# Performance work log

Hardware: AMD Instinct MI355X
Metric: run time of the kernel (lower is better)

The kernel has to match this reference:

```python
import jax, jax.numpy as jnp
import numpy as np

KS = 3
N = KS * KS
LN_EPS = 1e-5


def conv2d(x, w, stride=1, pad=0):
    return jax.lax.conv_general_dilated(
        x, w, (stride, stride), [(pad, pad), (pad, pad)],
        dimension_numbers=('NCHW', 'OIHW', 'NCHW'))


def layer_norm(x, g, b):
    mu = jnp.mean(x, axis=-1, keepdims=True)
    var = jnp.mean(jnp.square(x - mu), axis=-1, keepdims=True)
    return (x - mu) * jax.lax.rsqrt(var + LN_EPS) * g + b


def l2norm(x):
    n = jnp.sqrt(jnp.sum(jnp.square(x), axis=-1, keepdims=True))
    return x / jnp.maximum(n, 1e-12)


def deform_conv(x, w_p, b_p, w_d):
    # canonical DeformConv2d (kernel 3, pad 1, stride 1, no modulation)
    B, C, H, W = x.shape
    off = conv2d(x, w_p, stride=1, pad=1) + b_p[None, :, None, None]  # [B,2N,H,W]
    xp = jnp.pad(x, ((0, 0), (0, 0), (1, 1), (1, 1)))
    Hp, Wp = H + 2, W + 2
    pn = jnp.stack(jnp.meshgrid(jnp.arange(-1, 2), jnp.arange(-1, 2), indexing='ij'), 0)
    pn = pn.reshape(2, N).astype(x.dtype)  # kernel offsets, row-major (dx,dy)
    p0x = jnp.arange(1, H + 1, dtype=x.dtype)
    p0y = jnp.arange(1, W + 1, dtype=x.dtype)
    # sampling coords, [B,H,W,N]
    px = off[:, :N].transpose(0, 2, 3, 1) + p0x[None, :, None, None] + pn[0][None, None, None, :]
    py = off[:, N:].transpose(0, 2, 3, 1) + p0y[None, None, :, None] + pn[1][None, None, None, :]
    fx = jnp.floor(px)
    fy = jnp.floor(py)
    qlx = jnp.clip(fx, 0, Hp - 1)
    qly = jnp.clip(fy, 0, Wp - 1)
    qrx = jnp.clip(fx + 1, 0, Hp - 1)
    qry = jnp.clip(fy + 1, 0, Wp - 1)
    pxc = jnp.clip(px, 0, Hp - 1)
    pyc = jnp.clip(py, 0, Wp - 1)
    g_lt = (1 + (qlx - pxc)) * (1 + (qly - pyc))
    g_rb = (1 - (qrx - pxc)) * (1 - (qry - pyc))
    g_lb = (1 + (qlx - pxc)) * (1 - (qry - pyc))
    g_rt = (1 - (qrx - pxc)) * (1 + (qly - pyc))
    xf = xp.reshape(B, C, Hp * Wp)

    def gat(ix, iy):
        idx = (ix.astype(jnp.int32) * Wp + iy.astype(jnp.int32)).reshape(B, 1, -1)
        g = jnp.take_along_axis(xf, jnp.broadcast_to(idx, (B, C, idx.shape[-1])), axis=2)
        return g.reshape(B, C, H, W, N)

    xo = (g_lt[:, None] * gat(qlx, qly) + g_rb[:, None] * gat(qrx, qry)
          + g_lb[:, None] * gat(qlx, qry) + g_rt[:, None] * gat(qrx, qly))
    # [B,C,H,W,N] -> [B,C,H*ks,W*ks] (row = h*ks+kr, col = w*ks+kc)
    xo = xo.reshape(B, C, H, W, KS, KS).transpose(0, 1, 2, 4, 3, 5).reshape(B, C, H * KS, W * KS)
    return conv2d(xo, w_d, stride=KS, pad=0)


def setup_inputs() -> dict:
    key = jax.random.key(0)
    ks = jax.random.split(key, 8)
    B, C, H, W, heads = 4, 192, 64, 64, 6
    hid = 4 * C
    return {
        'x': jax.random.normal(ks[0], (B, C, H, W), dtype=jnp.float32),
        'gamma1': jnp.ones((C,), jnp.float32),
        'beta1': jnp.zeros((C,), jnp.float32),
        'gamma2': jnp.ones((C,), jnp.float32),
        'beta2': jnp.zeros((C,), jnp.float32),
        'temperature': jnp.ones((heads, 1, 1), jnp.float32),
        'w_qkv': jax.random.normal(ks[1], (3 * C, C), jnp.float32) * 0.02,
        'w_proj': jax.random.normal(ks[2], (C, C), jnp.float32) * 0.02,
        'w_p': jax.random.normal(ks[3], (2 * N, C, KS, KS), jnp.float32) * 0.01,
        'b_p': jnp.zeros((2 * N,), jnp.float32),
        'w_d': jax.random.normal(ks[4], (C, C, KS, KS), jnp.float32) * 0.02,
        'w_fc1': jax.random.normal(ks[5], (C, hid), jnp.float32) * 0.02,
        'b_fc1': jnp.zeros((hid,), jnp.float32),
        'w_fc2': jax.random.normal(ks[6], (hid, C), jnp.float32) * 0.02,
        'b_fc2': jnp.zeros((C,), jnp.float32),
    }


def reference(x, gamma1, beta1, gamma2, beta2, temperature, w_qkv, w_proj,
              w_p, b_p, w_d, w_fc1, b_fc1, w_fc2, b_fc2):
    B, C, H, W = x.shape
    heads = temperature.shape[0]
    xs = x.reshape(B, C, H * W).transpose(0, 2, 1)  # [B,HW,C]
    shortcut = xs
    xn = layer_norm(xs, gamma1, beta1).transpose(0, 2, 1).reshape(B, C, H, W)
    # SSA: deformable-conv query + channel attention over C
    q = deform_conv(xn, w_p, b_p, w_d)
    qkv = jnp.einsum('bchw,oc->bohw', xn, w_qkv)
    k_spe, v_spe = qkv[:, C:2 * C], qkv[:, 2 * C:]

    def split(t):
        return t.reshape(B, heads, C // heads, H * W)

    qh = split(q)
    kh = l2norm(split(k_spe))
    vh = l2norm(split(v_spe))
    attn = jnp.einsum('bhcn,bhdn->bhcd', qh, kh) * temperature[None]
    attn = jax.nn.softmax(attn, axis=-1)
    out = jnp.einsum('bhcd,bhdn->bhcn', attn, vh).reshape(B, C, H, W)
    out = jnp.einsum('bchw,oc->bohw', out, w_proj)
    xs2 = shortcut + out.reshape(B, C, H * W).transpose(0, 2, 1)
    h1 = layer_norm(xs2, gamma2, beta2)
    m = jax.nn.gelu(h1 @ w_fc1 + b_fc1, approximate=False) @ w_fc2 + b_fc2
    xs3 = xs2 + m
    return xs3.transpose(0, 2, 1).reshape(B, C, H, W)
```

## Files before the change

### kernel.cpp

```cpp
#include <hip/hip_runtime.h>
#include <math.h>

typedef unsigned short u16;
typedef unsigned int u32;
typedef short s16x8 __attribute__((ext_vector_type(8)));
typedef float f32x4 __attribute__((ext_vector_type(4)));

#define AS1 __attribute__((address_space(1)))
#define AS3 __attribute__((address_space(3)))

__device__ __forceinline__ float bf2f(u16 u) {
    union { u32 i; float f; } v; v.i = ((u32)u) << 16; return v.f;
}
__device__ __forceinline__ u16 f2bf(float f) {
    union { float f; u32 i; } v; v.f = f;
    u32 r = v.i + 0x7fffu + ((v.i >> 16) & 1u);
    return (u16)(r >> 16);
}
__device__ __forceinline__ void gll16(const u16* g, u16* l) {
    __builtin_amdgcn_global_load_lds((const AS1 u32*)g, (AS3 u32*)l, 16, 0, 0);
}

__global__ void prep_kernel(const float* __restrict__ wd, const float* __restrict__ wqkv,
                            const float* __restrict__ wfc1, const float* __restrict__ wfc2,
                            const float* __restrict__ wp,
                            u16* __restrict__ wdT, u16* __restrict__ wkvT,
                            u16* __restrict__ wf1T, u16* __restrict__ wf2T,
                            u16* __restrict__ wpT)
{
    int i = blockIdx.x * 256 + threadIdx.x;
    if (i < 331776) {
        int o = i / 1728, r = i % 1728;
        int p = r / 192, c = r % 192;
        int cs = c ^ ((o & 7) << 3);
        wdT[(p * 192 + o) * 192 + cs] = f2bf(wd[(o * 192 + c) * 9 + p]);
    }
    if (i < 73728) {
        int o = i / 192, c = i % 192;
        wkvT[i] = f2bf(wqkv[(192 + o) * 192 + c]);
    }
    if (i < 147456) {
        int n = i / 192, c = i % 192;
        wf1T[i] = f2bf(wfc1[c * 768 + n]);
        int n2 = i / 768, hh = i % 768;
        wf2T[i] = f2bf(wfc2[hh * 192 + n2]);
    }
    if (i < 31104) {
        int n = i / 1728, r = i % 1728;
        int p = r / 192, c = r % 192;
        wpT[i] = f2bf(wp[(n * 192 + c) * 9 + p]);
    } else if (i < 55296) {
        wpT[i] = 0;
    }
}

__global__ __launch_bounds__(256) void ln1_kernel(const float* __restrict__ x,
                                                  const float* __restrict__ g,
                                                  const float* __restrict__ be,
                                                  u16* __restrict__ xn)
{
    __shared__ float red0[256], red1[256];
    __shared__ float mu_s[64], rs_s[64];
    __shared__ float xt[64 * 193];
    __shared__ u16 tile[64 * 194];
    int t = threadIdx.x, tl = t & 63, cg = t >> 6;
    int m0 = blockIdx.x * 64;
    int b = m0 >> 12, hw0 = m0 & 4095;
    const float* xb = x + (size_t)b * 786432 + hw0 + tl;
    float s = 0.f, s2 = 0.f;
    for (int cc = cg; cc < 192; cc += 4) {
        float v = xb[cc * 4096];
        xt[tl * 193 + cc] = v;
        s += v; s2 += v * v;
    }
    red0[t] = s; red1[t] = s2;
    __syncthreads();
    if (t < 64) {
        float a = red0[t] + red0[64 + t] + red0[128 + t] + red0[192 + t];
        float q = red1[t] + red1[64 + t] + red1[128 + t] + red1[192 + t];
        float mu = a * (1.f / 192.f);
        float var = q * (1.f / 192.f) - mu * mu;
        mu_s[t] = mu; rs_s[t] = rsqrtf(var + 1e-5f);
    }
    __syncthreads();
    float mu = mu_s[tl], rs = rs_s[tl];
    for (int cc = cg; cc < 192; cc += 4) {
        float v = (xt[tl * 193 + cc] - mu) * rs * g[cc] + be[cc];
        tile[tl * 194 + cc] = f2bf(v);
    }
    __syncthreads();
    u32* dst = (u32*)(xn + (size_t)m0 * 192);
    for (int i = t; i < 64 * 96; i += 256) {
        int r = i / 96, c2 = i % 96;
        dst[i] = *(const u32*)&tile[r * 194 + c2 * 2];
    }
}

__global__ __launch_bounds__(256) void offconv_kernel(const u16* __restrict__ xn,
                                                      const u16* __restrict__ wpT,
                                                      const float* __restrict__ bp,
                                                      float* __restrict__ off)
{
    __shared__ u16 As[64 * 200];
    __shared__ u16 Bs[32 * 200];
    int bh = blockIdx.x;
    int b = bh >> 6, h = bh & 63;
    int t = threadIdx.x;
    int lane = t & 63, wv = t >> 6;
    f32x4 acc[2];
#pragma unroll
    for (int j = 0; j < 2; j++) { acc[j][0] = 0.f; acc[j][1] = 0.f; acc[j][2] = 0.f; acc[j][3] = 0.f; }
    int r = t >> 2, cq = (t & 3) * 48;
    for (int p = 0; p < 9; p++) {
        int dh = p / 3 - 1, dw = p % 3 - 1;
        int hr = h + dh, wr = r + dw;
        bool valid = (hr >= 0) && (hr < 64) && (wr >= 0) && (wr < 64);
        const u16* src = xn + ((size_t)(b * 4096 + hr * 64 + wr)) * 192 + cq;
#pragma unroll
        for (int j = 0; j < 6; j++) {
            s16x8 v = {0, 0, 0, 0, 0, 0, 0, 0};
            if (valid) v = *(const s16x8*)(src + j * 8);
            *(s16x8*)&As[r * 200 + cq + j * 8] = v;
        }
#pragma unroll
        for (int i = 0; i < 3; i++) {
            int q = t + i * 256;
            int n = q / 24, c8 = q % 24;
            *(s16x8*)&Bs[n * 200 + c8 * 8] =
                *(const s16x8*)(wpT + n * 1728 + p * 192 + c8 * 8);
        }
        __syncthreads();
#pragma unroll
        for (int kc = 0; kc < 6; kc++) {
            s16x8 af = *(const s16x8*)&As[(wv * 16 + (lane & 15)) * 200 + kc * 32 + (lane >> 4) * 8];
            s16x8 b0 = *(const s16x8*)&Bs[(lane & 15) * 200 + kc * 32 + (lane >> 4) * 8];
            s16x8 b1 = *(const s16x8*)&Bs[(16 + (lane & 15)) * 200 + kc * 32 + (lane >> 4) * 8];
            acc[0] = __builtin_amdgcn_mfma_f32_16x16x32_bf16(af, b0, acc[0], 0, 0, 0);
            acc[1] = __builtin_amdgcn_mfma_f32_16x16x32_bf16(af, b1, acc[1], 0, 0, 0);
        }
        __syncthreads();
    }
    int col = lane & 15;
    int wbase = wv * 16 + (lane >> 4) * 4;
#pragma unroll
    for (int j = 0; j < 2; j++) {
        int n = j * 16 + col;
        if (n < 18) {
            float bb = bp[n];
#pragma unroll
            for (int rr = 0; rr < 4; rr++) {
                int w = wbase + rr;
                off[((size_t)(b * 4096 + h * 64 + w)) * 18 + n] = acc[j][rr] + bb;
            }
        }
    }
}

__global__ __launch_bounds__(512, 2) void gemm_deform(const u16* __restrict__ xn,
                                                      const float* __restrict__ off,
                                                      const u16* __restrict__ wdT,
                                                      u16* __restrict__ qt)
{
    __shared__ u16 As[64 * 200];
    __shared__ u16 Bs[192 * 192];
    __shared__ int sidx[64][9][4];
    __shared__ float swt[64][9][4];
    int t = threadIdx.x, lane = t & 63, wv = t >> 6;
    int wm = wv & 1, wn = wv >> 1;
    int m0 = blockIdx.x * 64;
    int b = m0 >> 12;
    for (int i = t; i < 576; i += 512) {
        int mi = i / 9, p = i % 9;
        int m = m0 + mi;
        int hw = m & 4095;
        int h = hw >> 6, w = hw & 63;
        float ox = off[(size_t)m * 18 + p];
        float oy = off[(size_t)m * 18 + 9 + p];
        float px = ox + (float)(h + 1) + (float)(p / 3 - 1);
        float py = oy + (float)(w + 1) + (float)(p % 3 - 1);
        float fx = floorf(px), fy = floorf(py);
        float qlx = fminf(fmaxf(fx, 0.f), 65.f);
        float qly = fminf(fmaxf(fy, 0.f), 65.f);
        float qrx = fminf(fmaxf(fx + 1.f, 0.f), 65.f);
        float qry = fminf(fmaxf(fy + 1.f, 0.f), 65.f);
        float pxc = fminf(fmaxf(px, 0.f), 65.f);
        float pyc = fminf(fmaxf(py, 0.f), 65.f);
        float gxl = 1.f + (qlx - pxc), gxr = 1.f - (qrx - pxc);
        float gyl = 1.f + (qly - pyc), gyr = 1.f - (qry - pyc);
        int xl = (int)qlx, xr = (int)qrx, yl = (int)qly, yr = (int)qry;
        int cx[4] = {xl, xr, xl, xr};
        int cy[4] = {yl, yr, yr, yl};
        float cw[4] = {gxl * gyl, gxr * gyr, gxl * gyr, gxr * gyl};
#pragma unroll
        for (int k = 0; k < 4; k++) {
            bool ok = (cx[k] >= 1) && (cx[k] <= 64) && (cy[k] >= 1) && (cy[k] <= 64);
            sidx[mi][p][k] = ok ? (b * 4096 + (cx[k] - 1) * 64 + (cy[k] - 1)) * 192 : 0;
            swt[mi][p][k] = ok ? cw[k] : 0.f;
        }
    }
    __syncthreads();
    f32x4 acc[2][3];
#pragma unroll
    for (int i = 0; i < 2; i++)
#pragma unroll
        for (int j = 0; j < 3; j++) {
            acc[i][j][0] = 0.f; acc[i][j][1] = 0.f; acc[i][j][2] = 0.f; acc[i][j][3] = 0.f;
        }
    int mi = t >> 3, ch = (t & 7) * 24;
    int orow[3], oxr[3];
#pragma unroll
    for (int j = 0; j < 3; j++) {
        int o = wn * 48 + j * 16 + (lane & 15);
        orow[j] = o * 192;
        oxr[j] = (o & 7) << 3;
    }
    int kb0 = (lane >> 4) * 8;

    {
        const u16* bsrc = wdT;
#pragma unroll
        for (int i2 = 0; i2 < 9; i2++) {
            int jc = wv + 8 * i2;
            gll16(bsrc + jc * 512 + lane * 8, Bs + jc * 512);
        }
        const int*   si = sidx[mi][0];
        const float* sw = swt[mi][0];
        s16x8 pc[4][3];
#pragma unroll
        for (int k = 0; k < 4; k++)
#pragma unroll
            for (int s = 0; s < 3; s++)
                pc[k][s] = *(const s16x8*)(xn + si[k] + ch + s * 8);
        float v[24];
#pragma unroll
        for (int j = 0; j < 24; j++) v[j] = 0.f;
#pragma unroll
        for (int k = 0; k < 4; k++) {
            float wt = sw[k];
#pragma unroll
            for (int j = 0; j < 24; j++) v[j] += wt * bf2f((u16)pc[k][j >> 3][j & 7]);
        }
#pragma unroll
        for (int s = 0; s < 3; s++) {
            s16x8 ov;
#pragma unroll
            for (int e = 0; e < 8; e++) ov[e] = (short)f2bf(v[s * 8 + e]);
            *(s16x8*)&As[mi * 200 + ch + s * 8] = ov;
        }
        asm volatile("s_waitcnt vmcnt(0)" ::: "memory");
        __syncthreads();
    }

    for (int p = 0; p < 9; p++) {
        s16x8 nc[4][3];
        if (p < 8) {
            const int* si = sidx[mi][p + 1];
#pragma unroll
            for (int k = 0; k < 4; k++)
#pragma unroll
                for (int s = 0; s < 3; s++)
                    nc[k][s] = *(const s16x8*)(xn + si[k] + ch + s * 8);
        }
#pragma unroll
        for (int kk = 0; kk < 6; kk++) {
            int kb = kk * 32 + kb0;
            s16x8 af[2], bfr[3];
#pragma unroll
            for (int i = 0; i < 2; i++)
                af[i] = *(const s16x8*)&As[(wm * 32 + i * 16 + (lane & 15)) * 200 + kb];
#pragma unroll
            for (int j = 0; j < 3; j++)
                bfr[j] = *(const s16x8*)&Bs[orow[j] + (kb ^ oxr[j])];
#pragma unroll
            for (int i = 0; i < 2; i++)
#pragma unroll
                for (int j = 0; j < 3; j++)
                    acc[i][j] = __builtin_amdgcn_mfma_f32_16x16x32_bf16(af[i], bfr[j], acc[i][j], 0, 0, 0);
        }
        if (p < 8) {
            __syncthreads();
            const u16* bsrc = wdT + (size_t)(p + 1) * 36864;
#pragma unroll
            for (int i2 = 0; i2 < 9; i2++) {
                int jc = wv + 8 * i2;
                gll16(bsrc + jc * 512 + lane * 8, Bs + jc * 512);
            }
            const float* sw = swt[mi][p + 1];
            float v[24];
#pragma unroll
            for (int j = 0; j < 24; j++) v[j] = 0.f;
#pragma unroll
            for (int k = 0; k < 4; k++) {
                float wt = sw[k];
#pragma unroll
                for (int j = 0; j < 24; j++) v[j] += wt * bf2f((u16)nc[k][j >> 3][j & 7]);
            }
#pragma unroll
            for (int s = 0; s < 3; s++) {
                s16x8 ov;
#pragma unroll
                for (int e = 0; e < 8; e++) ov[e] = (short)f2bf(v[s * 8 + e]);
                *(s16x8*)&As[mi * 200 + ch + s * 8] = ov;
            }
            asm volatile("s_waitcnt vmcnt(0)" ::: "memory");
            __syncthreads();
        }
    }
    int col = lane & 15;
#pragma unroll
    for (int i = 0; i < 2; i++)
#pragma unroll
        for (int j = 0; j < 3; j++) {
            int mm = m0 + wm * 32 + i * 16 + (lane >> 4) * 4;
            int nn = wn * 48 + j * 16 + col;
#pragma unroll
            for (int r = 0; r < 4; r++)
                qt[(size_t)(mm + r) * 192 + nn] = f2bf(acc[i][j][r]);
        }
}

template<int BM, int BN, int WM, int WN, int EP>
__global__ __launch_bounds__((BM / WM) * (BN / WN) * 64)
void gemm_bt(const u16* __restrict__ A, int lda,
             const u16* __restrict__ B, int ldb, int bstride,
             void* __restrict__ out, int ldc,
             const float* __restrict__ ex1, int K)
{
    constexpr int BK = 32;
    constexpr int WAVES_M = BM / WM, WAVES_N = BN / WN, NW = WAVES_M * WAVES_N;
    constexpr int TM = WM / 16, TN = WN / 16;
    constexpr int NLA = BM / 16, NLB = BN / 16;
    __shared__ u16 As[BM * BK];
    __shared__ u16 Bs[BN * BK];
    int tid = threadIdx.x;
    int lane = tid & 63, wv = tid >> 6;
    int wm = wv % WAVES_M, wn = wv / WAVES_M;
    int m0 = blockIdx.x * BM, n0 = blockIdx.y * BN;
    const u16* Bp = B + (size_t)(m0 >> 12) * bstride;
    f32x4 acc[TM][TN];
#pragma unroll
    for (int i = 0; i < TM; i++)
#pragma unroll
        for (int j = 0; j < TN; j++) {
            acc[i][j][0] = 0.f; acc[i][j][1] = 0.f; acc[i][j][2] = 0.f; acc[i][j][3] = 0.f;
        }
    int arow_l = lane >> 2;
    int acol_l = (lane & 3) * 8;
    for (int k0 = 0; k0 < K; k0 += BK) {
#pragma unroll 1
        for (int j = wv; j < NLA + NLB; j += NW) {
            if (j < NLA) {
                int row = j * 16 + arow_l;
                gll16(A + (size_t)(m0 + row) * lda + k0 + acol_l, As + j * 512);
            } else {
                int row = (j - NLA) * 16 + arow_l;
                gll16(Bp + (size_t)(n0 + row) * ldb + k0 + acol_l, Bs + (j - NLA) * 512);
            }
        }
        asm volatile("s_waitcnt vmcnt(0)" ::: "memory");
        __syncthreads();
        s16x8 af[TM], bfr[TN];
#pragma unroll
        for (int i = 0; i < TM; i++)
            af[i] = *(const s16x8*)&As[(wm * WM + i * 16 + (lane & 15)) * BK + (lane >> 4) * 8];
#pragma unroll
        for (int j = 0; j < TN; j++)
            bfr[j] = *(const s16x8*)&Bs[(wn * WN + j * 16 + (lane & 15)) * BK + (lane >> 4) * 8];
#pragma unroll
        for (int i = 0; i < TM; i++)
#pragma unroll
            for (int j = 0; j < TN; j++)
                acc[i][j] = __builtin_amdgcn_mfma_f32_16x16x32_bf16(af[i], bfr[j], acc[i][j], 0, 0, 0);
        __syncthreads();
    }
    int col = lane & 15;
#pragma unroll
    for (int i = 0; i < TM; i++)
#pragma unroll
        for (int j = 0; j < TN; j++) {
            int mm = m0 + wm * WM + i * 16 + (lane >> 4) * 4;
            int nn = n0 + wn * WN + j * 16 + col;
            if (EP == 0) {
                u16* o = (u16*)out;
#pragma unroll
                for (int r = 0; r < 4; r++) o[(size_t)(mm + r) * ldc + nn] = f2bf(acc[i][j][r]);
            } else if (EP == 1) {
                float* o = (float*)out;
                const float* xr = ex1 + (size_t)(mm >> 12) * 786432 + (size_t)nn * 4096 + (mm & 4095);
#pragma unroll
                for (int r = 0; r < 4; r++) o[(size_t)(mm + r) * ldc + nn] = acc[i][j][r] + xr[r];
            } else if (EP == 2) {
                u16* o = (u16*)out;
                float bb = ex1[nn];
#pragma unroll
                for (int r = 0; r < 4; r++) {
                    float v = acc[i][j][r] + bb;
                    o[(size_t)(mm + r) * ldc + nn] = f2bf(0.5f * v * (1.f + erff(v * 0.70710678118654752f)));
                }
            } else {
                float* o = (float*)out;
                float bb = ex1[nn];
#pragma unroll
                for (int r = 0; r < 4; r++) o[(size_t)(mm + r) * ldc + nn] = acc[i][j][r] + bb;
            }
        }
}

__global__ __launch_bounds__(384) void norm_kernel(const u16* __restrict__ kv,
                                                   float* __restrict__ norm2)
{
    int b = blockIdx.y, ch = blockIdx.x;
    int t = threadIdx.x;
    const u16* base = kv + ((size_t)(b * 4096 + ch * 128)) * 384 + t;
    float s = 0.f;
    for (int r = 0; r < 128; r++) { float v = bf2f(base[(size_t)r * 384]); s += v * v; }
    atomicAdd(&norm2[b * 384 + t], s);
}

__global__ __launch_bounds__(64) void attnp_kernel(const u16* __restrict__ qt,
                                                   const u16* __restrict__ kvt,
                                                   float* __restrict__ raw)
{
    __shared__ float qT[32 * 69];
    __shared__ float kT[32 * 69];
    int ch = blockIdx.x, h = blockIdx.y, b = blockIdx.z;
    int t = threadIdx.x;
    size_t base = (size_t)(b * 4096 + ch * 64);
    for (int e = t; e < 2048; e += 64) {
        int r = e >> 5, c = e & 31;
        qT[c * 69 + r] = bf2f(qt[(base + r) * 192 + h * 32 + c]);
        kT[c * 69 + r] = bf2f(kvt[(base + r) * 384 + h * 32 + c]);
    }
    __syncthreads();
    int tc = t >> 3, td = t & 7;
    int c0 = tc * 4, d0 = td * 4;
    float acc[4][4] = {};
    for (int r = 0; r < 64; r++) {
        float qv[4], kv4[4];
#pragma unroll
        for (int u = 0; u < 4; u++) { qv[u] = qT[(c0 + u) * 69 + r]; kv4[u] = kT[(d0 + u) * 69 + r]; }
#pragma unroll
        for (int u = 0; u < 4; u++)
#pragma unroll
            for (int v = 0; v < 4; v++) acc[u][v] += qv[u] * kv4[v];
    }
    float* dst = raw + ((size_t)(b * 6 + h)) * 1024;
#pragma unroll
    for (int u = 0; u < 4; u++)
#pragma unroll
        for (int v = 0; v < 4; v++)
            atomicAdd(&dst[(c0 + u) * 32 + d0 + v], acc[u][v]);
}

__global__ __launch_bounds__(1024) void softmax_kernel(const float* __restrict__ raw,
                                                       const float* __restrict__ norm2,
                                                       const float* __restrict__ temp,
                                                       float* __restrict__ att2)
{
    int h = blockIdx.x, b = blockIdx.y;
    int t = threadIdx.x;
    int c = t >> 5, d = t & 31;
    __shared__ float invk[32], invv[32];
    if (t < 32)       invk[t] = 1.f / fmaxf(sqrtf(norm2[b * 384 + h * 32 + t]), 1e-12f);
    else if (t < 64)  invv[t - 32] = 1.f / fmaxf(sqrtf(norm2[b * 384 + 192 + h * 32 + (t - 32)]), 1e-12f);
    __syncthreads();
    float T = temp[h];
    float v = raw[((size_t)(b * 6 + h) * 32 + c) * 32 + d] * invk[d] * T;
    float mx = v;
    for (int s = 16; s > 0; s >>= 1) mx = fmaxf(mx, __shfl_xor(mx, s, 32));
    float e = expf(v - mx);
    float sm = e;
    for (int s = 16; s > 0; s >>= 1) sm += __shfl_xor(sm, s, 32);
    att2[((size_t)(b * 6 + h) * 32 + c) * 32 + d] = (e / sm) * invv[d];
}

__global__ __launch_bounds__(192) void mb_kernel(const float* __restrict__ wproj,
                                                 const float* __restrict__ att2,
                                                 u16* __restrict__ Mb)
{
    int o2 = blockIdx.x, b = blockIdx.y, t = threadIdx.x;
    int h = t >> 5, d = t & 31;
    float s = 0.f;
#pragma unroll
    for (int c = 0; c < 32; c++)
        s += wproj[o2 * 192 + h * 32 + c] * att2[((size_t)(b * 6 + h) * 32 + c) * 32 + d];
    Mb[((size_t)b * 192 + o2) * 192 + t] = f2bf(s);
}

__global__ __launch_bounds__(256) void ln2_kernel(const float* __restrict__ xs2,
                                                  const float* __restrict__ g,
                                                  const float* __restrict__ be,
                                                  u16* __restrict__ h1)
{
    int t = threadIdx.x;
    int wv = t >> 6, l = t & 63;
    size_t m = (size_t)blockIdx.x * 4 + wv;
    const float* row = xs2 + m * 192;
    float v0 = row[l], v1 = row[l + 64], v2 = row[l + 128];
    float s = v0 + v1 + v2, s2 = v0 * v0 + v1 * v1 + v2 * v2;
    for (int sh = 32; sh > 0; sh >>= 1) { s += __shfl_xor(s, sh); s2 += __shfl_xor(s2, sh); }
    float mu = s * (1.f / 192.f);
    float var = s2 * (1.f / 192.f) - mu * mu;
    float rs = rsqrtf(var + 1e-5f);
    u16* o = h1 + m * 192;
    o[l]       = f2bf((v0 - mu) * rs * g[l]       + be[l]);
    o[l + 64]  = f2bf((v1 - mu) * rs * g[l + 64]  + be[l + 64]);
    o[l + 128] = f2bf((v2 - mu) * rs * g[l + 128] + be[l + 128]);
}

__global__ __launch_bounds__(256) void final_kernel(const float* __restrict__ xs2,
                                                    const float* __restrict__ m2,
                                                    float* __restrict__ out)
{
    __shared__ float tile[192 * 65];
    int blk = blockIdx.x;
    int b = blk >> 6, hw0 = (blk & 63) * 64;
    int t = threadIdx.x;
    size_t mbase = ((size_t)b * 4096 + hw0) * 192;
    for (int i = t; i < 64 * 192; i += 256) {
        int r = i / 192, c = i % 192;
        tile[c * 65 + r] = xs2[mbase + i] + m2[mbase + i];
    }
    __syncthreads();
    for (int i = t; i < 64 * 192; i += 256) {
        int c = i / 64, r = i % 64;
        out[(size_t)b * 786432 + (size_t)c * 4096 + hw0 + r] = tile[c * 65 + r];
    }
}

extern "C" void kernel_launch(void* const* d_in, const int* in_sizes, int n_in,
                              void* d_out, int out_size, void* d_ws, size_t ws_size,
                              hipStream_t stream)
{
    const float* x      = (const float*)d_in[0];
    const float* gamma1 = (const float*)d_in[1];
    const float* beta1  = (const float*)d_in[2];
    const float* gamma2 = (const float*)d_in[3];
    const float* beta2  = (const float*)d_in[4];
    const float* temp   = (const float*)d_in[5];
    const float* w_qkv  = (const float*)d_in[6];
    const float* w_proj = (const float*)d_in[7];
    const float* w_p    = (const float*)d_in[8];
    const float* b_p    = (const float*)d_in[9];
    const float* w_d    = (const float*)d_in[10];
    const float* w_fc1  = (const float*)d_in[11];
    const float* b_fc1  = (const float*)d_in[12];
    const float* w_fc2  = (const float*)d_in[13];
    const float* b_fc2  = (const float*)d_in[14];
    float* out = (float*)d_out;
    char* ws = (char*)d_ws;

    u16*   xn    = (u16*)(ws + 0);
    float* off   = (float*)(ws + 6291456);
    u16*   adef  = (u16*)(ws + 7471104);
    u16*   wpT   = adef;
    u16*   m1    = adef;
    float* m2    = (float*)(ws + 7471104 + 25165824);
    u16*   qt    = (u16*)(ws + 64094208);
    u16*   kvt   = (u16*)(ws + 70385664);
    float* norm2 = (float*)(ws + 82968576);
    float* araw  = (float*)(ws + 82974720);
    float* att2  = (float*)(ws + 83073024);
    u16*   Mb    = (u16*)(ws + 83171328);
    float* xs2   = (float*)(ws + 83318784);
    u16*   h1    = xn;
    u16*   wdT   = (u16*)(ws + 95901696);
    u16*   wkvT  = (u16*)(ws + 96565248);
    u16*   wf1T  = (u16*)(ws + 96712704);
    u16*   wf2T  = (u16*)(ws + 97007616);

    hipMemsetAsync(norm2, 0, 6144 + 98304, stream);
    prep_kernel<<<1296, 256, 0, stream>>>(w_d, w_qkv, w_fc1, w_fc2, w_p, wdT, wkvT, wf1T, wf2T, wpT);
    ln1_kernel<<<256, 256, 0, stream>>>(x, gamma1, beta1, xn);
    offconv_kernel<<<256, 256, 0, stream>>>(xn, wpT, b_p, off);
    gemm_deform<<<256, 512, 0, stream>>>(xn, off, wdT, qt);
    gemm_bt<128, 128, 64, 64, 0><<<dim3(128, 3), 256, 0, stream>>>(xn, 192, wkvT, 192, 0, kvt, 384, nullptr, 192);
    norm_kernel<<<dim3(32, 4), 384, 0, stream>>>(kvt, norm2);
    attnp_kernel<<<dim3(64, 6, 4), 64, 0, stream>>>(qt, kvt, araw);
    softmax_kernel<<<dim3(6, 4), 1024, 0, stream>>>(araw, norm2, temp, att2);
    mb_kernel<<<dim3(192, 4), 192, 0, stream>>>(w_proj, att2, Mb);
    gemm_bt<128, 192, 64, 48, 1><<<dim3(128, 1), 512, 0, stream>>>(kvt + 192, 384, Mb, 192, 192 * 192, xs2, 192, x, 192);
    ln2_kernel<<<4096, 256, 0, stream>>>(xs2, gamma2, beta2, h1);
    gemm_bt<128, 128, 64, 64, 2><<<dim3(128, 6), 256, 0, stream>>>(h1, 192, wf1T, 192, 0, m1, 768, b_fc1, 192);
    gemm_bt<128, 192, 64, 48, 3><<<dim3(128, 1), 512, 0, stream>>>(m1, 768, wf2T, 768, 0, m2, 192, b_fc2, 768);
    final_kernel<<<256, 256, 0, stream>>>(xs2, m2, out);
}
```

Before: 270.3 us.

## Fuse norm, LayerNorm2 and final residual/transposes into GEMM epilogues; drop attention atomics

Folds the k/v squared-norm reduction into the kv GEMM epilogue and LayerNorm2 into the projection GEMM epilogue, which now uses a 64x192 tile so each block holds whole rows. The fc2 GEMM epilogue adds the residual and writes the NCHW output directly, removing the separate norm, ln2 and final transpose kernels and the m2 buffer. attnp now writes per-chunk partials instead of using atomics, and softmax sums the 64 partials. This saves launches and round trips through global memory, at the cost of heavier epilogues, strided output writes and extra partial-buffer traffic.

After: 244.3 us. 1.11x faster.

```diff
diff --git a/kernel.cpp b/kernel.cpp
--- a/kernel.cpp
+++ b/kernel.cpp
@@ -324,7 +324,10 @@
 void gemm_bt(const u16* __restrict__ A, int lda,
              const u16* __restrict__ B, int ldb, int bstride,
              void* __restrict__ out, int ldc,
-             const float* __restrict__ ex1, int K)
+             const float* __restrict__ ex1, int K,
+             const float* __restrict__ ex2,
+             const float* __restrict__ exg, const float* __restrict__ exb,
+             void* __restrict__ out2)
 {
     constexpr int BK = 32;
     constexpr int WAVES_M = BM / WM, WAVES_N = BN / WN, NW = WAVES_M * WAVES_N;
@@ -374,47 +377,142 @@
         __syncthreads();
     }
     int col = lane & 15;
-#pragma unroll
-    for (int i = 0; i < TM; i++)
-#pragma unroll
-        for (int j = 0; j < TN; j++) {
-            int mm = m0 + wm * WM + i * 16 + (lane >> 4) * 4;
-            int nn = n0 + wn * WN + j * 16 + col;
-            if (EP == 0) {
-                u16* o = (u16*)out;
+    int rg = lane >> 4;
+    if constexpr (EP == 0) {
+        u16* o = (u16*)out;
+#pragma unroll
+        for (int i = 0; i < TM; i++)
+#pragma unroll
+            for (int j = 0; j < TN; j++) {
+                int mm = m0 + wm * WM + i * 16 + rg * 4;
+                int nn = n0 + wn * WN + j * 16 + col;
 #pragma unroll
                 for (int r = 0; r < 4; r++) o[(size_t)(mm + r) * ldc + nn] = f2bf(acc[i][j][r]);
-            } else if (EP == 1) {
-                float* o = (float*)out;
-                const float* xr = ex1 + (size_t)(mm >> 12) * 786432 + (size_t)nn * 4096 + (mm & 4095);
-#pragma unroll
-                for (int r = 0; r < 4; r++) o[(size_t)(mm + r) * ldc + nn] = acc[i][j][r] + xr[r];
-            } else if (EP == 2) {
-                u16* o = (u16*)out;
+            }
+    } else if constexpr (EP == 2) {
+        u16* o = (u16*)out;
+#pragma unroll
+        for (int i = 0; i < TM; i++)
+#pragma unroll
+            for (int j = 0; j < TN; j++) {
+                int mm = m0 + wm * WM + i * 16 + rg * 4;
+                int nn = n0 + wn * WN + j * 16 + col;
                 float bb = ex1[nn];
 #pragma unroll
                 for (int r = 0; r < 4; r++) {
                     float v = acc[i][j][r] + bb;
                     o[(size_t)(mm + r) * ldc + nn] = f2bf(0.5f * v * (1.f + erff(v * 0.70710678118654752f)));
                 }
-            } else {
-                float* o = (float*)out;
+            }
+    } else if constexpr (EP == 4) {
+        __shared__ float lnA[BM][2];
+        __shared__ float lnB[BM][2];
+        float v[TM][TN][4];
+        float sr[TM][4], sq[TM][4];
+#pragma unroll
+        for (int i = 0; i < TM; i++)
+#pragma unroll
+            for (int r = 0; r < 4; r++) { sr[i][r] = 0.f; sq[i][r] = 0.f; }
+#pragma unroll
+        for (int i = 0; i < TM; i++) {
+            int mm = m0 + wm * WM + i * 16 + rg * 4;
+#pragma unroll
+            for (int j = 0; j < TN; j++) {
+                int nn = n0 + wn * WN + j * 16 + col;
+                const float* xr = ex1 + (size_t)(mm >> 12) * 786432 + (size_t)nn * 4096 + (mm & 4095);
+#pragma unroll
+                for (int r = 0; r < 4; r++) {
+                    float vv = acc[i][j][r] + xr[r];
+                    v[i][j][r] = vv;
+                    sr[i][r] += vv; sq[i][r] += vv * vv;
+                }
+            }
+        }
+#pragma unroll
+        for (int i = 0; i < TM; i++)
+#pragma unroll
+            for (int r = 0; r < 4; r++)
+#pragma unroll
+                for (int sh = 1; sh < 16; sh <<= 1) {
+                    sr[i][r] += __shfl_xor(sr[i][r], sh);
+                    sq[i][r] += __shfl_xor(sq[i][r], sh);
+                }
+        if (col == 0) {
+#pragma unroll
+            for (int i = 0; i < TM; i++)
+#pragma unroll
+                for (int r = 0; r < 4; r++) {
+                    int row = wm * WM + i * 16 + rg * 4 + r;
+                    lnA[row][wn] = sr[i][r];
+                    lnB[row][wn] = sq[i][r];
+                }
+        }
+        __syncthreads();
+        float* oxs = (float*)out;
+        u16* oh = (u16*)out2;
+#pragma unroll
+        for (int i = 0; i < TM; i++) {
+            int mm = m0 + wm * WM + i * 16 + rg * 4;
+#pragma unroll
+            for (int r = 0; r < 4; r++) {
+                int row = wm * WM + i * 16 + rg * 4 + r;
+                float tot = lnA[row][0] + lnA[row][1];
+                float tq  = lnB[row][0] + lnB[row][1];
+                float mu = tot * (1.f / 192.f);
+                float var = tq * (1.f / 192.f) - mu * mu;
+                float rstd = rsqrtf(var + 1e-5f);
+#pragma unroll
+                for (int j = 0; j < TN; j++) {
+                    int nn = n0 + wn * WN + j * 16 + col;
+                    float vv = v[i][j][r];
+                    oxs[(size_t)(mm + r) * ldc + nn] = vv;
+                    oh[(size_t)(mm + r) * ldc + nn] = f2bf((vv - mu) * rstd * exg[nn] + exb[nn]);
+                }
+            }
+        }
+    } else if constexpr (EP == 5) {
+        float* o = (float*)out;
+#pragma unroll
+        for (int i = 0; i < TM; i++)
+#pragma unroll
+            for (int j = 0; j < TN; j++) {
+                int mm = m0 + wm * WM + i * 16 + rg * 4;
+                int nn = n0 + wn * WN + j * 16 + col;
                 float bb = ex1[nn];
-#pragma unroll
-                for (int r = 0; r < 4; r++) o[(size_t)(mm + r) * ldc + nn] = acc[i][j][r] + bb;
-            }
-        }
-}
-
-__global__ __launch_bounds__(384) void norm_kernel(const u16* __restrict__ kv,
-                                                   float* __restrict__ norm2)
-{
-    int b = blockIdx.y, ch = blockIdx.x;
-    int t = threadIdx.x;
-    const u16* base = kv + ((size_t)(b * 4096 + ch * 128)) * 384 + t;
-    float s = 0.f;
-    for (int r = 0; r < 128; r++) { float v = bf2f(base[(size_t)r * 384]); s += v * v; }
-    atomicAdd(&norm2[b * 384 + t], s);
+                size_t obase = (size_t)(mm >> 12) * 786432 + (size_t)nn * 4096;
+#pragma unroll
+                for (int r = 0; r < 4; r++) {
+                    float vv = acc[i][j][r] + bb + ex2[(size_t)(mm + r) * ldc + nn];
+                    o[obase + ((mm + r) & 4095)] = vv;
+                }
+            }
+    } else if constexpr (EP == 6) {
+        u16* o = (u16*)out;
+        float* nrm = (float*)out2;
+        int bI = m0 >> 12;
+#pragma unroll
+        for (int j = 0; j < TN; j++) {
+            float s = 0.f;
+#pragma unroll
+            for (int i = 0; i < TM; i++) {
+                int mm = m0 + wm * WM + i * 16 + rg * 4;
+                int nn = n0 + wn * WN + j * 16 + col;
+#pragma unroll
+                for (int r = 0; r < 4; r++) {
+                    u16 hb = f2bf(acc[i][j][r]);
+                    o[(size_t)(mm + r) * ldc + nn] = hb;
+                    float fv = bf2f(hb);
+                    s += fv * fv;
+                }
+            }
+            s += __shfl_xor(s, 16);
+            s += __shfl_xor(s, 32);
+            if (rg == 0) {
+                int nn = n0 + wn * WN + j * 16 + col;
+                atomicAdd(&nrm[bI * 384 + nn], s);
+            }
+        }
+    }
 }
 
 __global__ __launch_bounds__(64) void attnp_kernel(const u16* __restrict__ qt,
@@ -444,12 +542,12 @@
 #pragma unroll
             for (int v = 0; v < 4; v++) acc[u][v] += qv[u] * kv4[v];
     }
-    float* dst = raw + ((size_t)(b * 6 + h)) * 1024;
+    float* dst = raw + (((size_t)(b * 6 + h) * 64 + ch) * 1024);
 #pragma unroll
     for (int u = 0; u < 4; u++)
 #pragma unroll
         for (int v = 0; v < 4; v++)
-            atomicAdd(&dst[(c0 + u) * 32 + d0 + v], acc[u][v]);
+            dst[(c0 + u) * 32 + d0 + v] = acc[u][v];
 }
 
 __global__ __launch_bounds__(1024) void softmax_kernel(const float* __restrict__ raw,
@@ -465,7 +563,11 @@
     else if (t < 64)  invv[t - 32] = 1.f / fmaxf(sqrtf(norm2[b * 384 + 192 + h * 32 + (t - 32)]), 1e-12f);
     __syncthreads();
     float T = temp[h];
-    float v = raw[((size_t)(b * 6 + h) * 32 + c) * 32 + d] * invk[d] * T;
+    const float* pr = raw + (size_t)(b * 6 + h) * 65536 + c * 32 + d;
+    float v = 0.f;
+#pragma unroll
+    for (int ch = 0; ch < 64; ch++) v += pr[ch * 1024];
+    v *= invk[d] * T;
     float mx = v;
     for (int s = 16; s > 0; s >>= 1) mx = fmaxf(mx, __shfl_xor(mx, s, 32));
     float e = expf(v - mx);
@@ -485,47 +587,6 @@
     for (int c = 0; c < 32; c++)
         s += wproj[o2 * 192 + h * 32 + c] * att2[((size_t)(b * 6 + h) * 32 + c) * 32 + d];
     Mb[((size_t)b * 192 + o2) * 192 + t] = f2bf(s);
-}
-
-__global__ __launch_bounds__(256) void ln2_kernel(const float* __restrict__ xs2,
-                                                  const float* __restrict__ g,
-                                                  const float* __restrict__ be,
-                                                  u16* __restrict__ h1)
-{
-    int t = threadIdx.x;
-    int wv = t >> 6, l = t & 63;
-    size_t m = (size_t)blockIdx.x * 4 + wv;
-    const float* row = xs2 + m * 192;
-    float v0 = row[l], v1 = row[l + 64], v2 = row[l + 128];
-    float s = v0 + v1 + v2, s2 = v0 * v0 + v1 * v1 + v2 * v2;
-    for (int sh = 32; sh > 0; sh >>= 1) { s += __shfl_xor(s, sh); s2 += __shfl_xor(s2, sh); }
-    float mu = s * (1.f / 192.f);
-    float var = s2 * (1.f / 192.f) - mu * mu;
-    float rs = rsqrtf(var + 1e-5f);
-    u16* o = h1 + m * 192;
-    o[l]       = f2bf((v0 - mu) * rs * g[l]       + be[l]);
-    o[l + 64]  = f2bf((v1 - mu) * rs * g[l + 64]  + be[l + 64]);
-    o[l + 128] = f2bf((v2 - mu) * rs * g[l + 128] + be[l + 128]);
-}
-
-__global__ __launch_bounds__(256) void final_kernel(const float* __restrict__ xs2,
-                                                    const float* __restrict__ m2,
-                                                    float* __restrict__ out)
-{
-    __shared__ float tile[192 * 65];
-    int blk = blockIdx.x;
-    int b = blk >> 6, hw0 = (blk & 63) * 64;
-    int t = threadIdx.x;
-    size_t mbase = ((size_t)b * 4096 + hw0) * 192;
-    for (int i = t; i < 64 * 192; i += 256) {
-        int r = i / 192, c = i % 192;
-        tile[c * 65 + r] = xs2[mbase + i] + m2[mbase + i];
-    }
-    __syncthreads();
-    for (int i = t; i < 64 * 192; i += 256) {
-        int c = i / 64, r = i % 64;
-        out[(size_t)b * 786432 + (size_t)c * 4096 + hw0 + r] = tile[c * 65 + r];
-    }
 }
 
 extern "C" void kernel_launch(void* const* d_in, const int* in_sizes, int n_in,
@@ -555,11 +616,10 @@
     u16*   adef  = (u16*)(ws + 7471104);
     u16*   wpT   = adef;
     u16*   m1    = adef;
-    float* m2    = (float*)(ws + 7471104 + 25165824);
+    float* araw  = (float*)(ws + 32636928);
     u16*   qt    = (u16*)(ws + 64094208);
     u16*   kvt   = (u16*)(ws + 70385664);
     float* norm2 = (float*)(ws + 82968576);
-    float* araw  = (float*)(ws + 82974720);
     float* att2  = (float*)(ws + 83073024);
     u16*   Mb    = (u16*)(ws + 83171328);
     float* xs2   = (float*)(ws + 83318784);
@@ -569,19 +629,20 @@
     u16*   wf1T  = (u16*)(ws + 96712704);
     u16*   wf2T  = (u16*)(ws + 97007616);
 
-    hipMemsetAsync(norm2, 0, 6144 + 98304, stream);
+    hipMemsetAsync(norm2, 0, 6144, stream);
     prep_kernel<<<1296, 256, 0, stream>>>(w_d, w_qkv, w_fc1, w_fc2, w_p, wdT, wkvT, wf1T, wf2T, wpT);
     ln1_kernel<<<256, 256, 0, stream>>>(x, gamma1, beta1, xn);
     offconv_kernel<<<256, 256, 0, stream>>>(xn, wpT, b_p, off);
     gemm_deform<<<256, 512, 0, stream>>>(xn, off, wdT, qt);
-    gemm_bt<128, 128, 64, 64, 0><<<dim3(128, 3), 256, 0, stream>>>(xn, 192, wkvT, 192, 0, kvt, 384, nullptr, 192);
-    norm_kernel<<<dim3(32, 4), 384, 0, stream>>>(kvt, norm2);
+    gemm_bt<128, 128, 64, 64, 6><<<dim3(128, 3), 256, 0, stream>>>(
+        xn, 192, wkvT, 192, 0, kvt, 384, nullptr, 192, nullptr, nullptr, nullptr, norm2);
     attnp_kernel<<<dim3(64, 6, 4), 64, 0, stream>>>(qt, kvt, araw);
     softmax_kernel<<<dim3(6, 4), 1024, 0, stream>>>(araw, norm2, temp, att2);
     mb_kernel<<<dim3(192, 4), 192, 0, stream>>>(w_proj, att2, Mb);
-    gemm_bt<128, 192, 64, 48, 1><<<dim3(128, 1), 512, 0, stream>>>(kvt + 192, 384, Mb, 192, 192 * 192, xs2, 192, x, 192);
-    ln2_kernel<<<4096, 256, 0, stream>>>(xs2, gamma2, beta2, h1);
-    gemm_bt<128, 128, 64, 64, 2><<<dim3(128, 6), 256, 0, stream>>>(h1, 192, wf1T, 192, 0, m1, 768, b_fc1, 192);
-    gemm_bt<128, 192, 64, 48, 3><<<dim3(128, 1), 512, 0, stream>>>(m1, 768, wf2T, 768, 0, m2, 192, b_fc2, 768);
-    final_kernel<<<256, 256, 0, stream>>>(xs2, m2, out);
-}
+    gemm_bt<64, 192, 32, 96, 4><<<dim3(256, 1), 256, 0, stream>>>(
+        kvt + 192, 384, Mb, 192, 192 * 192, xs2, 192, x, 192, nullptr, gamma2, beta2, h1);
+    gemm_bt<128, 128, 64, 64, 2><<<dim3(128, 6), 256, 0, stream>>>(
+        h1, 192, wf1T, 192, 0, m1, 768, b_fc1, 192, nullptr, nullptr, nullptr, nullptr);
+    gemm_bt<128, 96, 64, 48, 5><<<dim3(128, 2), 256, 0, stream>>>(
+        m1, 768, wf2T, 768, 0, out, 192, b_fc2, 768, xs2, nullptr, nullptr, nullptr);
+}
```
